# Optimization experiments

Hardware: AMD Instinct MI355X
Metric: run time of the kernel (lower is better)

Reference implementation:

```python
import jax, jax.numpy as jnp
import numpy as np

N_NODES = 100000
N_EDGES = 3200000
D_FEAT = 128
HIDDEN = 16
N_CLASSES = 7


def gcn_conv(x, edge_index, edge_weight, W, b, n_nodes):
    h = x @ W  # dense projection first (Fout small)
    src, dst = edge_index[0], edge_index[1]
    # add self-loops with weight 1
    loop = jnp.arange(n_nodes, dtype=edge_index.dtype)
    src_a = jnp.concatenate([src, loop])
    dst_a = jnp.concatenate([dst, loop])
    ew_a = jnp.concatenate([edge_weight, jnp.ones((n_nodes,), dtype=x.dtype)])
    deg = jax.ops.segment_sum(ew_a, dst_a, num_segments=n_nodes)
    dinv = jnp.where(deg > 0, jax.lax.rsqrt(deg), 0.0)
    norm = dinv[src_a] * ew_a * dinv[dst_a]  # [E+N]
    msg = h[src_a] * norm[:, None]  # gather + scale
    out = jax.ops.segment_sum(msg, dst_a, num_segments=n_nodes)
    return out + b


def setup_inputs() -> dict:
    key = jax.random.key(0)
    k = jax.random.split(key, 8)
    x = jax.random.normal(k[0], (N_NODES, D_FEAT), dtype=jnp.float32)
    edge_index = jax.random.randint(k[1], (2, N_EDGES), 0, N_NODES, dtype=jnp.int64)
    edge_weight = jax.random.uniform(k[2], (N_EDGES,), dtype=jnp.float32)
    s1 = 1.0 / np.sqrt(D_FEAT)
    s2 = 1.0 / np.sqrt(HIDDEN)
    W1 = jax.random.uniform(k[3], (D_FEAT, HIDDEN), jnp.float32, -s1, s1)
    b1 = jnp.zeros((HIDDEN,), jnp.float32)
    W2 = jax.random.uniform(k[4], (HIDDEN, N_CLASSES), jnp.float32, -s2, s2)
    b2 = jnp.zeros((N_CLASSES,), jnp.float32)
    return {"x": x, "edge_index": edge_index, "edge_weight": edge_weight,
            "W1": W1, "b1": b1, "W2": W2, "b2": b2}


def reference(x, edge_index, edge_weight, W1, b1, W2, b2):
    h = jax.nn.relu(gcn_conv(x, edge_index, edge_weight, W1, b1, N_NODES))
    out = gcn_conv(h, edge_index, edge_weight, W2, b2, N_NODES)
    return jax.nn.log_softmax(out, axis=1)
```

## Files before the change

kernel.cpp:

```cpp
#include <hip/hip_runtime.h>
#include <hip/hip_fp16.h>
#include <math.h>

constexpr int NN = 100000;
constexpr int NE = 3200000;
constexpr int DF = 128;
constexpr int NH = 16;
constexpr int NC = 7;

constexpr int BN    = 256;
constexpr int NB    = (NN + BN - 1) / BN;
constexpr int CAP   = 9216;
constexpr int CHUNK = 4096;
constexpr int AB    = (NE + CHUNK - 1) / CHUNK;
constexpr int EPT   = CHUNK / 1024;
constexpr int SPT   = (CAP + 1023) / 1024;

constexpr float QS   = 32767.0f;
constexpr float QINV = 1.0f / 32767.0f;

typedef _Float16 half8 __attribute__((ext_vector_type(8)));
typedef float    f32x4 __attribute__((ext_vector_type(4)));

__global__ void k_zero(int* __restrict__ gcur) {
    int t = blockIdx.x * blockDim.x + threadIdx.x;
    if (t < NB) gcur[t] = 0;
}

__global__ void __launch_bounds__(1024)
k_append(const int* __restrict__ src,
         const int* __restrict__ dst,
         const float* __restrict__ w,
         int* __restrict__ gcur,
         uint2* __restrict__ ebuf) {
    __shared__ int hist[NB];
    __shared__ int cscan[512];
    __shared__ int basev[NB];
    __shared__ uint2 staged[CHUNK];
    __shared__ unsigned short sbkt[CHUNK];
    for (int i = threadIdx.x; i < NB; i += 1024) hist[i] = 0;
    __syncthreads();
    int e0 = blockIdx.x * CHUNK;
    unsigned slo[EPT], sw[EPT];
    int sbr[EPT];
#pragma unroll
    for (int k = 0; k < EPT; ++k) {
        int e = e0 + (int)threadIdx.x + k * 1024;
        sbr[k] = -1;
        if (e < NE) {
            int d = __builtin_nontemporal_load(dst + e);
            int b = d >> 8;
            int r = atomicAdd(&hist[b], 1);
            slo[k] = ((unsigned)(d & (BN - 1)) << 17) |
                     (unsigned)__builtin_nontemporal_load(src + e);
            sw[k]  = (unsigned)(__builtin_nontemporal_load(w + e) * QS + 0.5f);
            sbr[k] = (b << 13) | r;
        }
    }
    __syncthreads();
    {
        int v0 = (threadIdx.x < NB) ? hist[threadIdx.x] : 0;
        if (threadIdx.x < 512) cscan[threadIdx.x] = v0;
        __syncthreads();
        for (int off = 1; off < 512; off <<= 1) {
            int v = (threadIdx.x < 512 && threadIdx.x >= off) ? cscan[threadIdx.x - off] : 0;
            __syncthreads();
            if (threadIdx.x < 512) cscan[threadIdx.x] += v;
            __syncthreads();
        }
    }
    if (threadIdx.x < NB) {
        int c = hist[threadIdx.x];
        basev[threadIdx.x] = (c > 0) ? atomicAdd(&gcur[threadIdx.x], c) : 0;
    }
    __syncthreads();
#pragma unroll
    for (int k = 0; k < EPT; ++k) {
        if (sbr[k] >= 0) {
            int b = sbr[k] >> 13;
            int idx = (cscan[b] - hist[b]) + (sbr[k] & 0x1FFF);
            uint2 v; v.x = slo[k]; v.y = sw[k];
            staged[idx] = v;
            sbkt[idx] = (unsigned short)b;
        }
    }
    __syncthreads();
    int total = min(CHUNK, NE - e0);
    for (int i = threadIdx.x; i < total; i += 1024) {
        int b = sbkt[i];
        int st = cscan[b] - hist[b];
        int pos = basev[b] + (i - st);
        if (pos < CAP) ebuf[(size_t)b * CAP + pos] = staged[i];
    }
}

__global__ void __launch_bounds__(1024)
k_sort(const int* __restrict__ gcur,
       uint2* __restrict__ ebuf,
       int* __restrict__ rs,
       int* __restrict__ rc,
       float* __restrict__ dinv) {
    __shared__ int cursor[BN];
    __shared__ int scanS[BN];
    __shared__ int startEx[BN];
    __shared__ unsigned sorted[CAP];
    int b = blockIdx.x;
    int tid = threadIdx.x;
    int cnt = min(gcur[b], CAP);
    const uint2* eb = ebuf + (size_t)b * CAP;
    if (tid < BN) cursor[tid] = 0;
    __syncthreads();
    unsigned sval[SPT];
    int sdr[SPT];
#pragma unroll
    for (int k = 0; k < SPT; ++k) {
        int i = tid + k * 1024;
        sdr[k] = -1;
        if (i < cnt) {
            uint2 v = eb[i];
            int dl = (v.x >> 17) & (BN - 1);
            int r = atomicAdd(&cursor[dl], 1);
            sval[k] = (v.x & 0x1FFFF) | (v.y << 17);
            sdr[k] = (dl << 14) | r;
        }
    }
    __syncthreads();
    if (tid < BN) scanS[tid] = cursor[tid];
    __syncthreads();
    for (int off = 1; off < BN; off <<= 1) {
        int v = (tid < BN && tid >= off) ? scanS[tid - off] : 0;
        __syncthreads();
        if (tid < BN) scanS[tid] += v;
        __syncthreads();
    }
    if (tid < BN) {
        int ex = scanS[tid] - cursor[tid];
        startEx[tid] = ex;
        int n = b * BN + tid;
        if (n < NN) { rs[n] = b * CAP * 2 + ex; rc[n] = cursor[tid]; }
    }
    __syncthreads();
#pragma unroll
    for (int k = 0; k < SPT; ++k) {
        if (sdr[k] >= 0)
            sorted[startEx[sdr[k] >> 14] + (sdr[k] & 0x3FFF)] = sval[k];
    }
    __syncthreads();
    unsigned* eb32 = (unsigned*)ebuf + (size_t)b * CAP * 2;
    for (int i = tid; i < cnt; i += 1024) eb32[i] = sorted[i];
    {
        int node = tid >> 2, part = tid & 3;
        float s = (part == 0) ? 1.0f : 0.0f;
        int s0 = startEx[node], c = cursor[node];
        for (int i = part; i < c; i += 4) s += (float)(sorted[s0 + i] >> 17) * QINV;
        s += __shfl_xor(s, 1, 4);
        s += __shfl_xor(s, 2, 4);
        if (part == 0) {
            int n = b * BN + node;
            if (n < NN) dinv[n] = rsqrtf(s);
        }
    }
}

__global__ void __launch_bounds__(256)
k_proj1(const float* __restrict__ x,
        const float* __restrict__ W1,
        const float* __restrict__ dinv,
        __half* __restrict__ h1p) {
    int wave = threadIdx.x >> 6;
    int lane = threadIdx.x & 63;
    int tile = blockIdx.x * 4 + wave;
    if (tile * 16 >= NN) return;
    int m    = lane & 15;
    int quad = lane >> 4;
    half8 bfrag[4];
#pragma unroll
    for (int kc = 0; kc < 4; ++kc)
#pragma unroll
        for (int j = 0; j < 8; ++j)
            bfrag[kc][j] = (_Float16)W1[(kc * 32 + quad * 8 + j) * NH + m];
    int base = tile * 16;
    const float* xr = x + (size_t)(base + m) * DF + quad * 8;
    f32x4 acc = {0.f, 0.f, 0.f, 0.f};
#pragma unroll
    for (int kc = 0; kc < 4; ++kc) {
        const float4* p = (const float4*)(xr + kc * 32);
        float4 u0 = p[0];
        float4 u1 = p[1];
        half8 afrag;
        afrag[0] = (_Float16)u0.x; afrag[1] = (_Float16)u0.y;
        afrag[2] = (_Float16)u0.z; afrag[3] = (_Float16)u0.w;
        afrag[4] = (_Float16)u1.x; afrag[5] = (_Float16)u1.y;
        afrag[6] = (_Float16)u1.z; afrag[7] = (_Float16)u1.w;
        acc = __builtin_amdgcn_mfma_f32_16x16x32_f16(afrag, bfrag[kc], acc, 0, 0, 0);
    }
    float4 d4 = *(const float4*)(dinv + base + quad * 4);
#pragma unroll
    for (int reg = 0; reg < 4; ++reg) {
        float dd = (reg == 0) ? d4.x : (reg == 1) ? d4.y : (reg == 2) ? d4.z : d4.w;
        int row = quad * 4 + reg;
        h1p[(size_t)(base + row) * 16 + m] = __float2half(acc[reg] * dd);
    }
}

__global__ void __launch_bounds__(256)
k_agg1p(const int* __restrict__ rs,
        const int* __restrict__ rc,
        const unsigned* __restrict__ cbuf,
        const __half* __restrict__ h1p,
        const float* __restrict__ dinv,
        const float* __restrict__ b1,
        const float* __restrict__ W2,
        __half* __restrict__ h2p) {
    const uint2* hp4 = (const uint2*)h1p;
    int t = blockIdx.x * 256 + threadIdx.x;
    int n = t >> 2;
    int f4 = t & 3;
    if (n >= NN) return;
    float a0, a1, a2, a3;
    {
        uint2 u = hp4[n * 4 + f4];
        float2 lo = __half22float2(*(const __half2*)&u.x);
        float2 hi = __half22float2(*(const __half2*)&u.y);
        a0 = lo.x; a1 = lo.y; a2 = hi.x; a3 = hi.y;
    }
    int s0 = rs[n], c = rc[n];
    int i = 0;
    for (; i + 3 < c; i += 4) {
        unsigned e0 = cbuf[s0 + i];
        unsigned e1 = cbuf[s0 + i + 1];
        unsigned e2 = cbuf[s0 + i + 2];
        unsigned e3 = cbuf[s0 + i + 3];
        uint2 u0 = hp4[(e0 & 0x1FFFF) * 4 + f4];
        uint2 u1 = hp4[(e1 & 0x1FFFF) * 4 + f4];
        uint2 u2 = hp4[(e2 & 0x1FFFF) * 4 + f4];
        uint2 u3 = hp4[(e3 & 0x1FFFF) * 4 + f4];
        float w0 = (float)(e0 >> 17) * QINV;
        float w1 = (float)(e1 >> 17) * QINV;
        float w2 = (float)(e2 >> 17) * QINV;
        float w3 = (float)(e3 >> 17) * QINV;
        float2 l0 = __half22float2(*(const __half2*)&u0.x);
        float2 h0 = __half22float2(*(const __half2*)&u0.y);
        float2 l1 = __half22float2(*(const __half2*)&u1.x);
        float2 h1v = __half22float2(*(const __half2*)&u1.y);
        float2 l2 = __half22float2(*(const __half2*)&u2.x);
        float2 h2v = __half22float2(*(const __half2*)&u2.y);
        float2 l3 = __half22float2(*(const __half2*)&u3.x);
        float2 h3v = __half22float2(*(const __half2*)&u3.y);
        a0 += w0 * l0.x + w1 * l1.x + w2 * l2.x + w3 * l3.x;
        a1 += w0 * l0.y + w1 * l1.y + w2 * l2.y + w3 * l3.y;
        a2 += w0 * h0.x + w1 * h1v.x + w2 * h2v.x + w3 * h3v.x;
        a3 += w0 * h0.y + w1 * h1v.y + w2 * h2v.y + w3 * h3v.y;
    }
    for (; i < c; ++i) {
        unsigned e0 = cbuf[s0 + i];
        uint2 u0 = hp4[(e0 & 0x1FFFF) * 4 + f4];
        float w0 = (float)(e0 >> 17) * QINV;
        float2 l0 = __half22float2(*(const __half2*)&u0.x);
        float2 h0 = __half22float2(*(const __half2*)&u0.y);
        a0 += w0 * l0.x;
        a1 += w0 * l0.y;
        a2 += w0 * h0.x;
        a3 += w0 * h0.y;
    }
    float di = dinv[n];
    int fb = 4 * f4;
    float hr0 = fmaxf(di * a0 + b1[fb + 0], 0.0f);
    float hr1 = fmaxf(di * a1 + b1[fb + 1], 0.0f);
    float hr2 = fmaxf(di * a2 + b1[fb + 2], 0.0f);
    float hr3 = fmaxf(di * a3 + b1[fb + 3], 0.0f);
    float p0, p1, p2, p3, p4, p5, p6;
    {
        const float* w0r = W2 + (fb + 0) * NC;
        const float* w1r = W2 + (fb + 1) * NC;
        const float* w2r = W2 + (fb + 2) * NC;
        const float* w3r = W2 + (fb + 3) * NC;
        p0 = hr0 * w0r[0] + hr1 * w1r[0] + hr2 * w2r[0] + hr3 * w3r[0];
        p1 = hr0 * w0r[1] + hr1 * w1r[1] + hr2 * w2r[1] + hr3 * w3r[1];
        p2 = hr0 * w0r[2] + hr1 * w1r[2] + hr2 * w2r[2] + hr3 * w3r[2];
        p3 = hr0 * w0r[3] + hr1 * w1r[3] + hr2 * w2r[3] + hr3 * w3r[3];
        p4 = hr0 * w0r[4] + hr1 * w1r[4] + hr2 * w2r[4] + hr3 * w3r[4];
        p5 = hr0 * w0r[5] + hr1 * w1r[5] + hr2 * w2r[5] + hr3 * w3r[5];
        p6 = hr0 * w0r[6] + hr1 * w1r[6] + hr2 * w2r[6] + hr3 * w3r[6];
    }
#pragma unroll
    for (int mask = 1; mask < 4; mask <<= 1) {
        p0 += __shfl_xor(p0, mask, 4);
        p1 += __shfl_xor(p1, mask, 4);
        p2 += __shfl_xor(p2, mask, 4);
        p3 += __shfl_xor(p3, mask, 4);
        p4 += __shfl_xor(p4, mask, 4);
        p5 += __shfl_xor(p5, mask, 4);
        p6 += __shfl_xor(p6, mask, 4);
    }
    float pa = (f4 == 0) ? p0 : (f4 == 1) ? p2 : (f4 == 2) ? p4 : p6;
    float pb = (f4 == 0) ? p1 : (f4 == 1) ? p3 : (f4 == 2) ? p5 : 0.0f;
    __half2 hv;
    hv.x = __float2half(di * pa);
    hv.y = __float2half(di * pb);
    ((__half2*)h2p)[n * 4 + f4] = hv;
}

__global__ void __launch_bounds__(256)
k_agg2_lsm(const int* __restrict__ rs,
           const int* __restrict__ rc,
           const unsigned* __restrict__ cbuf,
           const __half* __restrict__ h2p,
           const float* __restrict__ dinv,
           const float* __restrict__ b2,
           float* __restrict__ out) {
    const uint2* hp2 = (const uint2*)h2p;
    int t = blockIdx.x * 256 + threadIdx.x;
    int n = t >> 1;
    int c2 = t & 1;
    if (n >= NN) return;
    float a0, a1, a2, a3;
    {
        uint2 u = hp2[n * 2 + c2];
        float2 lo = __half22float2(*(const __half2*)&u.x);
        float2 hi = __half22float2(*(const __half2*)&u.y);
        a0 = lo.x; a1 = lo.y; a2 = hi.x; a3 = hi.y;
    }
    int s0 = rs[n], c = rc[n];
    int i = 0;
    for (; i + 3 < c; i += 4) {
        unsigned e0 = cbuf[s0 + i];
        unsigned e1 = cbuf[s0 + i + 1];
        unsigned e2 = cbuf[s0 + i + 2];
        unsigned e3 = cbuf[s0 + i + 3];
        uint2 u0 = hp2[(e0 & 0x1FFFF) * 2 + c2];
        uint2 u1 = hp2[(e1 & 0x1FFFF) * 2 + c2];
        uint2 u2 = hp2[(e2 & 0x1FFFF) * 2 + c2];
        uint2 u3 = hp2[(e3 & 0x1FFFF) * 2 + c2];
        float w0 = (float)(e0 >> 17) * QINV;
        float w1 = (float)(e1 >> 17) * QINV;
        float w2 = (float)(e2 >> 17) * QINV;
        float w3 = (float)(e3 >> 17) * QINV;
        float2 l0 = __half22float2(*(const __half2*)&u0.x);
        float2 h0 = __half22float2(*(const __half2*)&u0.y);
        float2 l1 = __half22float2(*(const __half2*)&u1.x);
        float2 h1v = __half22float2(*(const __half2*)&u1.y);
        float2 l2 = __half22float2(*(const __half2*)&u2.x);
        float2 h2v = __half22float2(*(const __half2*)&u2.y);
        float2 l3 = __half22float2(*(const __half2*)&u3.x);
        float2 h3v = __half22float2(*(const __half2*)&u3.y);
        a0 += w0 * l0.x + w1 * l1.x + w2 * l2.x + w3 * l3.x;
        a1 += w0 * l0.y + w1 * l1.y + w2 * l2.y + w3 * l3.y;
        a2 += w0 * h0.x + w1 * h1v.x + w2 * h2v.x + w3 * h3v.x;
        a3 += w0 * h0.y + w1 * h1v.y + w2 * h2v.y + w3 * h3v.y;
    }
    for (; i < c; ++i) {
        unsigned e0 = cbuf[s0 + i];
        uint2 u0 = hp2[(e0 & 0x1FFFF) * 2 + c2];
        float w0 = (float)(e0 >> 17) * QINV;
        float2 l0 = __half22float2(*(const __half2*)&u0.x);
        float2 h0 = __half22float2(*(const __half2*)&u0.y);
        a0 += w0 * l0.x;
        a1 += w0 * l0.y;
        a2 += w0 * h0.x;
        a3 += w0 * h0.y;
    }
    float di = dinv[n];
    int cb = 4 * c2;
    float va0 = di * a0 + b2[cb + 0];
    float va1 = di * a1 + b2[cb + 1];
    float va2 = di * a2 + b2[cb + 2];
    float va3 = (c2 == 0) ? (di * a3 + b2[3]) : -1e30f;
    float m = fmaxf(fmaxf(va0, va1), fmaxf(va2, va3));
    m = fmaxf(m, __shfl_xor(m, 1, 2));
    float s = __expf(va0 - m) + __expf(va1 - m) + __expf(va2 - m) + __expf(va3 - m);
    s += __shfl_xor(s, 1, 2);
    float lse = m + __logf(s);
    int base = n * NC + cb;
    out[base + 0] = va0 - lse;
    out[base + 1] = va1 - lse;
    out[base + 2] = va2 - lse;
    if (c2 == 0) out[base + 3] = va3 - lse;
}

extern "C" void kernel_launch(void* const* d_in, const int* in_sizes, int n_in,
                              void* d_out, int out_size, void* d_ws, size_t ws_size,
                              hipStream_t stream) {
    const float* x  = (const float*)d_in[0];
    const int*   ei = (const int*)d_in[1];
    const float* ew = (const float*)d_in[2];
    const float* W1 = (const float*)d_in[3];
    const float* b1 = (const float*)d_in[4];
    const float* W2 = (const float*)d_in[5];
    const float* b2 = (const float*)d_in[6];
    float* out = (float*)d_out;

    const int* srcp = ei;
    const int* dstp = ei + NE;

    float*  ws   = (float*)d_ws;
    float*  dinv = ws;
    __half* h1p  = (__half*)(ws + 100352);
    __half* h2p  = (__half*)(ws + 900352);
    int*    gcur = (int*)(ws + 1300352);
    int*    rs   = (int*)(ws + 1301376);
    int*    rc   = (int*)(ws + 1401728);
    uint2*  ebuf = (uint2*)(ws + 1502080);
    const unsigned* cbuf = (const unsigned*)ebuf;

    auto cdiv = [](long long a, long long b) { return (int)((a + b - 1) / b); };

    k_zero<<<1, 1024, 0, stream>>>(gcur);
    k_append<<<AB, 1024, 0, stream>>>(srcp, dstp, ew, gcur, ebuf);
    k_sort<<<NB, 1024, 0, stream>>>(gcur, ebuf, rs, rc, dinv);
    k_proj1<<<cdiv(NN, 64), 256, 0, stream>>>(x, W1, dinv, h1p);
    k_agg1p<<<cdiv((long long)NN * 4, 256), 256, 0, stream>>>(rs, rc, cbuf, h1p, dinv, b1, W2, h2p);
    k_agg2_lsm<<<cdiv((long long)NN * 2, 256), 256, 0, stream>>>(rs, rc, cbuf, h2p, dinv, b2, out);
}
```

Measured before the change: 217.2 us.

## Use wavefront shuffle scans, pack bucket ids into staged entries, unroll gathers by eight

Replaces the shared-memory Hillis-Steele scans in the append and sort kernels with 64-lane wavefront shuffle scans plus a small cross-wave fixup, which removes many block-wide barriers. It packs the bucket id into the upper bits of the quantized weight word so the separate shared bucket array goes away, and the sort kernel masks those bits off. Both aggregation kernels gain an 8-way unrolled gather loop to keep more loads in flight, and the zeroing kernel becomes a hipMemsetAsync. These add register pressure and rely on the weight and bucket fields fitting in 32 bits.

```diff
diff --git a/kernel.cpp b/kernel.cpp
--- a/kernel.cpp
+++ b/kernel.cpp
@@ -21,11 +21,6 @@
 
 typedef _Float16 half8 __attribute__((ext_vector_type(8)));
 typedef float    f32x4 __attribute__((ext_vector_type(4)));
-
-__global__ void k_zero(int* __restrict__ gcur) {
-    int t = blockIdx.x * blockDim.x + threadIdx.x;
-    if (t < NB) gcur[t] = 0;
-}
 
 __global__ void __launch_bounds__(1024)
 k_append(const int* __restrict__ src,
@@ -36,8 +31,8 @@
     __shared__ int hist[NB];
     __shared__ int cscan[512];
     __shared__ int basev[NB];
+    __shared__ int wsum[8];
     __shared__ uint2 staged[CHUNK];
-    __shared__ unsigned short sbkt[CHUNK];
     for (int i = threadIdx.x; i < NB; i += 1024) hist[i] = 0;
     __syncthreads();
     int e0 = blockIdx.x * CHUNK;
@@ -53,22 +48,33 @@
             int r = atomicAdd(&hist[b], 1);
             slo[k] = ((unsigned)(d & (BN - 1)) << 17) |
                      (unsigned)__builtin_nontemporal_load(src + e);
-            sw[k]  = (unsigned)(__builtin_nontemporal_load(w + e) * QS + 0.5f);
+            unsigned q = (unsigned)(__builtin_nontemporal_load(w + e) * QS + 0.5f);
+            sw[k]  = ((unsigned)b << 15) | q;
             sbr[k] = (b << 13) | r;
         }
     }
     __syncthreads();
     {
-        int v0 = (threadIdx.x < NB) ? hist[threadIdx.x] : 0;
-        if (threadIdx.x < 512) cscan[threadIdx.x] = v0;
+        int v = 0;
+        if (threadIdx.x < 512) {
+            v = (threadIdx.x < NB) ? hist[threadIdx.x] : 0;
+#pragma unroll
+            for (int d = 1; d < 64; d <<= 1) {
+                int u = __shfl_up(v, d, 64);
+                if ((int)(threadIdx.x & 63) >= d) v += u;
+            }
+            if ((threadIdx.x & 63) == 63) wsum[threadIdx.x >> 6] = v;
+        }
         __syncthreads();
-        for (int off = 1; off < 512; off <<= 1) {
-            int v = (threadIdx.x < 512 && threadIdx.x >= off) ? cscan[threadIdx.x - off] : 0;
-            __syncthreads();
-            if (threadIdx.x < 512) cscan[threadIdx.x] += v;
-            __syncthreads();
-        }
-    }
+        if (threadIdx.x == 0) {
+            int acc = 0;
+#pragma unroll
+            for (int i = 0; i < 8; ++i) { int t = wsum[i]; wsum[i] = acc; acc += t; }
+        }
+        __syncthreads();
+        if (threadIdx.x < 512) cscan[threadIdx.x] = v + wsum[threadIdx.x >> 6];
+    }
+    __syncthreads();
     if (threadIdx.x < NB) {
         int c = hist[threadIdx.x];
         basev[threadIdx.x] = (c > 0) ? atomicAdd(&gcur[threadIdx.x], c) : 0;
@@ -81,16 +87,16 @@
             int idx = (cscan[b] - hist[b]) + (sbr[k] & 0x1FFF);
             uint2 v; v.x = slo[k]; v.y = sw[k];
             staged[idx] = v;
-            sbkt[idx] = (unsigned short)b;
         }
     }
     __syncthreads();
     int total = min(CHUNK, NE - e0);
     for (int i = threadIdx.x; i < total; i += 1024) {
-        int b = sbkt[i];
+        uint2 sv = staged[i];
+        int b = (int)(sv.y >> 15);
         int st = cscan[b] - hist[b];
         int pos = basev[b] + (i - st);
-        if (pos < CAP) ebuf[(size_t)b * CAP + pos] = staged[i];
+        if (pos < CAP) ebuf[(size_t)b * CAP + pos] = sv;
     }
 }
 
@@ -103,6 +109,7 @@
     __shared__ int cursor[BN];
     __shared__ int scanS[BN];
     __shared__ int startEx[BN];
+    __shared__ int wsum[4];
     __shared__ unsigned sorted[CAP];
     int b = blockIdx.x;
     int tid = threadIdx.x;
@@ -120,19 +127,32 @@
             uint2 v = eb[i];
             int dl = (v.x >> 17) & (BN - 1);
             int r = atomicAdd(&cursor[dl], 1);
-            sval[k] = (v.x & 0x1FFFF) | (v.y << 17);
+            sval[k] = (v.x & 0x1FFFF) | ((v.y & 0x7FFFu) << 17);
             sdr[k] = (dl << 14) | r;
         }
     }
     __syncthreads();
-    if (tid < BN) scanS[tid] = cursor[tid];
-    __syncthreads();
-    for (int off = 1; off < BN; off <<= 1) {
-        int v = (tid < BN && tid >= off) ? scanS[tid - off] : 0;
+    {
+        int v = 0;
+        if (tid < BN) {
+            v = cursor[tid];
+#pragma unroll
+            for (int d = 1; d < 64; d <<= 1) {
+                int u = __shfl_up(v, d, 64);
+                if ((tid & 63) >= d) v += u;
+            }
+            if ((tid & 63) == 63) wsum[tid >> 6] = v;
+        }
         __syncthreads();
-        if (tid < BN) scanS[tid] += v;
+        if (tid == 0) {
+            int acc = 0;
+#pragma unroll
+            for (int i = 0; i < 4; ++i) { int t = wsum[i]; wsum[i] = acc; acc += t; }
+        }
         __syncthreads();
-    }
+        if (tid < BN) scanS[tid] = v + wsum[tid >> 6];
+    }
+    __syncthreads();
     if (tid < BN) {
         int ex = scanS[tid] - cursor[tid];
         startEx[tid] = ex;
@@ -226,6 +246,56 @@
     }
     int s0 = rs[n], c = rc[n];
     int i = 0;
+    for (; i + 7 < c; i += 8) {
+        unsigned e0 = cbuf[s0 + i];
+        unsigned e1 = cbuf[s0 + i + 1];
+        unsigned e2 = cbuf[s0 + i + 2];
+        unsigned e3 = cbuf[s0 + i + 3];
+        unsigned e4 = cbuf[s0 + i + 4];
+        unsigned e5 = cbuf[s0 + i + 5];
+        unsigned e6 = cbuf[s0 + i + 6];
+        unsigned e7 = cbuf[s0 + i + 7];
+        uint2 u0 = hp4[(e0 & 0x1FFFF) * 4 + f4];
+        uint2 u1 = hp4[(e1 & 0x1FFFF) * 4 + f4];
+        uint2 u2 = hp4[(e2 & 0x1FFFF) * 4 + f4];
+        uint2 u3 = hp4[(e3 & 0x1FFFF) * 4 + f4];
+        uint2 u4 = hp4[(e4 & 0x1FFFF) * 4 + f4];
+        uint2 u5 = hp4[(e5 & 0x1FFFF) * 4 + f4];
+        uint2 u6 = hp4[(e6 & 0x1FFFF) * 4 + f4];
+        uint2 u7 = hp4[(e7 & 0x1FFFF) * 4 + f4];
+        float w0 = (float)(e0 >> 17) * QINV;
+        float w1 = (float)(e1 >> 17) * QINV;
+        float w2 = (float)(e2 >> 17) * QINV;
+        float w3 = (float)(e3 >> 17) * QINV;
+        float w4 = (float)(e4 >> 17) * QINV;
+        float w5 = (float)(e5 >> 17) * QINV;
+        float w6 = (float)(e6 >> 17) * QINV;
+        float w7 = (float)(e7 >> 17) * QINV;
+        float2 l0 = __half22float2(*(const __half2*)&u0.x);
+        float2 h0 = __half22float2(*(const __half2*)&u0.y);
+        float2 l1 = __half22float2(*(const __half2*)&u1.x);
+        float2 h1v = __half22float2(*(const __half2*)&u1.y);
+        float2 l2 = __half22float2(*(const __half2*)&u2.x);
+        float2 h2v = __half22float2(*(const __half2*)&u2.y);
+        float2 l3 = __half22float2(*(const __half2*)&u3.x);
+        float2 h3v = __half22float2(*(const __half2*)&u3.y);
+        float2 l4 = __half22float2(*(const __half2*)&u4.x);
+        float2 h4v = __half22float2(*(const __half2*)&u4.y);
+        float2 l5 = __half22float2(*(const __half2*)&u5.x);
+        float2 h5v = __half22float2(*(const __half2*)&u5.y);
+        float2 l6 = __half22float2(*(const __half2*)&u6.x);
+        float2 h6v = __half22float2(*(const __half2*)&u6.y);
+        float2 l7 = __half22float2(*(const __half2*)&u7.x);
+        float2 h7v = __half22float2(*(const __half2*)&u7.y);
+        a0 += w0 * l0.x + w1 * l1.x + w2 * l2.x + w3 * l3.x
+            + w4 * l4.x + w5 * l5.x + w6 * l6.x + w7 * l7.x;
+        a1 += w0 * l0.y + w1 * l1.y + w2 * l2.y + w3 * l3.y
+            + w4 * l4.y + w5 * l5.y + w6 * l6.y + w7 * l7.y;
+        a2 += w0 * h0.x + w1 * h1v.x + w2 * h2v.x + w3 * h3v.x
+            + w4 * h4v.x + w5 * h5v.x + w6 * h6v.x + w7 * h7v.x;
+        a3 += w0 * h0.y + w1 * h1v.y + w2 * h2v.y + w3 * h3v.y
+            + w4 * h4v.y + w5 * h5v.y + w6 * h6v.y + w7 * h7v.y;
+    }
     for (; i + 3 < c; i += 4) {
         unsigned e0 = cbuf[s0 + i];
         unsigned e1 = cbuf[s0 + i + 1];
@@ -323,6 +393,56 @@
     }
     int s0 = rs[n], c = rc[n];
     int i = 0;
+    for (; i + 7 < c; i += 8) {
+        unsigned e0 = cbuf[s0 + i];
+        unsigned e1 = cbuf[s0 + i + 1];
+        unsigned e2 = cbuf[s0 + i + 2];
+        unsigned e3 = cbuf[s0 + i + 3];
+        unsigned e4 = cbuf[s0 + i + 4];
+        unsigned e5 = cbuf[s0 + i + 5];
+        unsigned e6 = cbuf[s0 + i + 6];
+        unsigned e7 = cbuf[s0 + i + 7];
+        uint2 u0 = hp2[(e0 & 0x1FFFF) * 2 + c2];
+        uint2 u1 = hp2[(e1 & 0x1FFFF) * 2 + c2];
+        uint2 u2 = hp2[(e2 & 0x1FFFF) * 2 + c2];
+        uint2 u3 = hp2[(e3 & 0x1FFFF) * 2 + c2];
+        uint2 u4 = hp2[(e4 & 0x1FFFF) * 2 + c2];
+        uint2 u5 = hp2[(e5 & 0x1FFFF) * 2 + c2];
+        uint2 u6 = hp2[(e6 & 0x1FFFF) * 2 + c2];
+        uint2 u7 = hp2[(e7 & 0x1FFFF) * 2 + c2];
+        float w0 = (float)(e0 >> 17) * QINV;
+        float w1 = (float)(e1 >> 17) * QINV;
+        float w2 = (float)(e2 >> 17) * QINV;
+        float w3 = (float)(e3 >> 17) * QINV;
+        float w4 = (float)(e4 >> 17) * QINV;
+        float w5 = (float)(e5 >> 17) * QINV;
+        float w6 = (float)(e6 >> 17) * QINV;
+        float w7 = (float)(e7 >> 17) * QINV;
+        float2 l0 = __half22float2(*(const __half2*)&u0.x);
+        float2 h0 = __half22float2(*(const __half2*)&u0.y);
+        float2 l1 = __half22float2(*(const __half2*)&u1.x);
+        float2 h1v = __half22float2(*(const __half2*)&u1.y);
+        float2 l2 = __half22float2(*(const __half2*)&u2.x);
+        float2 h2v = __half22float2(*(const __half2*)&u2.y);
+        float2 l3 = __half22float2(*(const __half2*)&u3.x);
+        float2 h3v = __half22float2(*(const __half2*)&u3.y);
+        float2 l4 = __half22float2(*(const __half2*)&u4.x);
+        float2 h4v = __half22float2(*(const __half2*)&u4.y);
+        float2 l5 = __half22float2(*(const __half2*)&u5.x);
+        float2 h5v = __half22float2(*(const __half2*)&u5.y);
+        float2 l6 = __half22float2(*(const __half2*)&u6.x);
+        float2 h6v = __half22float2(*(const __half2*)&u6.y);
+        float2 l7 = __half22float2(*(const __half2*)&u7.x);
+        float2 h7v = __half22float2(*(const __half2*)&u7.y);
+        a0 += w0 * l0.x + w1 * l1.x + w2 * l2.x + w3 * l3.x
+            + w4 * l4.x + w5 * l5.x + w6 * l6.x + w7 * l7.x;
+        a1 += w0 * l0.y + w1 * l1.y + w2 * l2.y + w3 * l3.y
+            + w4 * l4.y + w5 * l5.y + w6 * l6.y + w7 * l7.y;
+        a2 += w0 * h0.x + w1 * h1v.x + w2 * h2v.x + w3 * h3v.x
+            + w4 * h4v.x + w5 * h5v.x + w6 * h6v.x + w7 * h7v.x;
+        a3 += w0 * h0.y + w1 * h1v.y + w2 * h2v.y + w3 * h3v.y
+            + w4 * h4v.y + w5 * h5v.y + w6 * h6v.y + w7 * h7v.y;
+    }
     for (; i + 3 < c; i += 4) {
         unsigned e0 = cbuf[s0 + i];
         unsigned e1 = cbuf[s0 + i + 1];
@@ -405,7 +525,7 @@
 
     auto cdiv = [](long long a, long long b) { return (int)((a + b - 1) / b); };
 
-    k_zero<<<1, 1024, 0, stream>>>(gcur);
+    hipMemsetAsync(gcur, 0, NB * sizeof(int), stream);
     k_append<<<AB, 1024, 0, stream>>>(srcp, dstp, ew, gcur, ebuf);
     k_sort<<<NB, 1024, 0, stream>>>(gcur, ebuf, rs, rc, dinv);
     k_proj1<<<cdiv(NN, 64), 256, 0, stream>>>(x, W1, dinv, h1p);
```

Result: no change. 213.2 us (-1.8%).
